# Optimization experiments

Hardware: AMD Instinct MI355X
Metric: run time of the kernel (lower is better)

The kernel has to match this reference:

```python
import jax, jax.numpy as jnp
import numpy as np

KH = KW = 3
PAD = 1
STRIDE = 1
C_IN = 32
C_OUT = 16
H = W = 64
B = 64
H_OUT = (H - KH + 2 * PAD) // STRIDE + 1
W_OUT = (W - KW + 2 * PAD) // STRIDE + 1
S = H_OUT * W_OUT
K = C_IN * KH * KW


def unfold_2d(x):
    # x: [B, C, H, W] -> [B, C*KH*KW, S], torch.nn.functional.unfold ordering
    xp = jnp.pad(x, ((0, 0), (0, 0), (PAD, PAD), (PAD, PAD)))
    patches = []
    for i in range(KH):
        for j in range(KW):
            patches.append(xp[:, :, i:i + H_OUT * STRIDE:STRIDE, j:j + W_OUT * STRIDE:STRIDE])
    u = jnp.stack(patches, axis=2)  # [B, C, KH*KW, H_OUT, W_OUT]
    return u.reshape(x.shape[0], K, S)


def setup_inputs() -> dict:
    key = jax.random.key(0)
    k1, k2, k3 = jax.random.split(key, 3)
    X = jax.random.normal(k1, (B, C_IN, H, W), dtype=jnp.float32)
    # kaiming normal (linear): std = 1/sqrt(fan_in), fan_in = K for each location's GEMM
    weight = jax.random.normal(k2, (S, K, C_OUT), dtype=jnp.float32) / jnp.sqrt(jnp.float32(K))
    # xavier uniform over [H_OUT, W_OUT]
    lim = np.sqrt(6.0 / (H_OUT + W_OUT))
    bias = jax.random.uniform(k3, (H_OUT, W_OUT), dtype=jnp.float32, minval=-lim, maxval=lim)
    return {"X": X, "weight": weight, "bias": bias}


def reference(X, weight, bias):
    ufld = unfold_2d(X)                               # [B, K, S]
    ufld = ufld + bias.reshape(1, 1, -1)              # bias added per-location to patches
    h = jnp.einsum('bks,skc->bcs', ufld, weight)      # per-location unshared GEMM
    return h.reshape(X.shape[0], C_OUT, H_OUT, W_OUT)
```

## Files before the change

### kernel.cpp

```cpp
#include <hip/hip_runtime.h>
#include <stdint.h>
#include <stddef.h>

#define HOUT 64
#define WOUT 64
#define CIN  32
#define COUT 16
#define SLOC 4096
#define KTOT 288
#define HPAD 66
#define WPAD 148

typedef __attribute__((ext_vector_type(8))) short  short8;
typedef __attribute__((ext_vector_type(4))) float  floatx4;
typedef __attribute__((ext_vector_type(2))) float  floatx2;

static __device__ __forceinline__ unsigned short f2bf(float f) {
    union { float f; unsigned int u; } v; v.f = f;
    unsigned int u = v.u;
    unsigned int r = (u + 0x7FFFu + ((u >> 16) & 1u)) >> 16;
    return (unsigned short)r;
}

__global__ __launch_bounds__(256) void prep_kernel(const float* __restrict__ X,
                                                   unsigned short* __restrict__ xt) {
    const int id  = blockIdx.x;
    const int tid = threadIdx.x;

    if (id < 260) {
        int h1, w1;
        if (id < 66)       { h1 = 0;  w1 = id; }
        else if (id < 132) { h1 = 65; w1 = id - 66; }
        else { int r = id - 132; h1 = (r >> 1) + 1; w1 = (r & 1) ? 65 : 0; }
        ((uint4*)(xt + (size_t)(h1 * HPAD + w1) * 2048))[tid] = uint4{0u, 0u, 0u, 0u};
    }

    const int w   = tid >> 2;
    const int cg8 = (tid & 3) * 8;
#pragma unroll
    for (int u = 0; u < 2; ++u) {
        const int unit = id * 2 + u;
        const int h = unit >> 6, b = unit & 63;
        const float* xb = X + (((size_t)b * CIN + cg8) * HOUT + h) * WOUT + w;
        unsigned short v[8];
#pragma unroll
        for (int j = 0; j < 8; ++j)
            v[j] = f2bf(xb[(size_t)j * HOUT * WOUT]);
        uint4 pack;
        pack.x = (unsigned)v[0] | ((unsigned)v[1] << 16);
        pack.y = (unsigned)v[2] | ((unsigned)v[3] << 16);
        pack.z = (unsigned)v[4] | ((unsigned)v[5] << 16);
        pack.w = (unsigned)v[6] | ((unsigned)v[7] << 16);
        *(uint4*)(xt + (size_t)((h + 1) * HPAD + (w + 1)) * 2048 + b * CIN + cg8) = pack;
    }
}

__global__ __launch_bounds__(256, 8) void varconv_kernel(const unsigned short* __restrict__ xt,
                                                         const float* __restrict__ Wg,
                                                         const float* __restrict__ bias,
                                                         float* __restrict__ out) {
    __shared__ __align__(16) unsigned int wru[2][16 * WPAD];
    __shared__ float cs[2][4][16];

    const int id   = blockIdx.x;
    const int sg   = (id & 7) * 256 + (id >> 3);
    const int s0   = sg * 2;
    const int y    = s0 >> 6;
    const int x0   = s0 & 63;
    const int tid  = threadIdx.x;
    const int lane = tid & 63;
    const int wv   = tid >> 6;
    const int q    = lane >> 4;
    const int n    = lane & 15;
    const int B0   = wv * 16;

    const uint4* wsrc = (const uint4*)(Wg + (size_t)s0 * (KTOT * COUT));
    float cacc0[4] = {0.f, 0.f, 0.f, 0.f};
    float cacc1[4] = {0.f, 0.f, 0.f, 0.f};

#define STTASK(T2, SITE, CACC)                                                 \
    {                                                                          \
        const int ng = (T2) & 3, cp = ((T2) >> 2) & 15, t = (T2) >> 6;         \
        const int kA = 18 * cp + t;                                            \
        union { uint4 u; float f[4]; } fA, fB;                                 \
        fA.u = wsrc[(SITE) * 1152 + kA * 4 + ng];                              \
        fB.u = wsrc[(SITE) * 1152 + (kA + 9) * 4 + ng];                        \
        unsigned int* wb = &wru[SITE][0];                                      \
        _Pragma("unroll")                                                      \
        for (int m = 0; m < 4; ++m) {                                          \
            CACC[m] += fA.f[m] + fB.f[m];                                      \
            wb[(4 * ng + m) * WPAD + t * 16 + cp] =                            \
                (unsigned)f2bf(fA.f[m]) | ((unsigned)f2bf(fB.f[m]) << 16);     \
        }                                                                      \
    }

#pragma unroll
    for (int it = 0; it < 5; ++it) {
        const int tau = tid + it * 256;
        if (tau < 576) {
            STTASK(tau, 0, cacc0)
        } else if (tau < 1152) {
            const int t2 = tau - 576;
            STTASK(t2, 1, cacc1)
        }
    }
#undef STTASK

#pragma unroll
    for (int m = 0; m < 4; ++m) {
        cacc0[m] += __shfl_xor(cacc0[m], 4, 64);
        cacc1[m] += __shfl_xor(cacc1[m], 4, 64);
        cacc0[m] += __shfl_xor(cacc0[m], 8, 64);
        cacc1[m] += __shfl_xor(cacc1[m], 8, 64);
        cacc0[m] += __shfl_xor(cacc0[m], 16, 64);
        cacc1[m] += __shfl_xor(cacc1[m], 16, 64);
        cacc0[m] += __shfl_xor(cacc0[m], 32, 64);
        cacc1[m] += __shfl_xor(cacc1[m], 32, 64);
    }
    if (lane < 4) {
#pragma unroll
        for (int m = 0; m < 4; ++m) {
            cs[0][wv][4 * lane + m] = cacc0[m];
            cs[1][wv][4 * lane + m] = cacc1[m];
        }
    }

    __syncthreads();

    floatx4 acc[2];
#pragma unroll
    for (int i = 0; i < 2; ++i) acc[i] = floatx4{0.f, 0.f, 0.f, 0.f};

#define COMPUTE(I)                                                             \
    {                                                                          \
        const int x = x0 + (I);                                                \
        short8 af[9], bf[9];                                                   \
        _Pragma("unroll")                                                      \
        for (int t = 0; t < 9; ++t) {                                          \
            const int cy = t / 3, cx = t % 3;                                  \
            af[t] = *(const short8*)(xt + (size_t)((y + cy) * HPAD + (x + cx)) * 2048 \
                                        + (B0 + n) * CIN + q * 8);             \
        }                                                                      \
        _Pragma("unroll")                                                      \
        for (int t = 0; t < 9; ++t)                                            \
            bf[t] = *(const short8*)&wru[I][n * WPAD + t * 16 + 4 * q];        \
        const float badd = bias[s0 + (I)] * (cs[I][0][n] + cs[I][1][n]        \
                                           + cs[I][2][n] + cs[I][3][n]);       \
        _Pragma("unroll")                                                      \
        for (int t = 0; t < 9; ++t)                                            \
            acc[I] = __builtin_amdgcn_mfma_f32_16x16x32_bf16(af[t], bf[t], acc[I], 0, 0, 0); \
        acc[I][0] += badd; acc[I][1] += badd;                                  \
        acc[I][2] += badd; acc[I][3] += badd;                                  \
    }

    COMPUTE(0)
    COMPUTE(1)
#undef COMPUTE

#pragma unroll
    for (int r = 0; r < 4; ++r) {
        const int b = B0 + 4 * q + r;
        float* dst = out + ((size_t)(b * COUT + n)) * SLOC + s0;
        *(floatx2*)dst = floatx2{acc[0][r], acc[1][r]};
    }
}

extern "C" void kernel_launch(void* const* d_in, const int* in_sizes, int n_in,
                              void* d_out, int out_size, void* d_ws, size_t ws_size,
                              hipStream_t stream) {
    const float* X    = (const float*)d_in[0];
    const float* Wg   = (const float*)d_in[1];
    const float* bias = (const float*)d_in[2];
    float* out = (float*)d_out;

    unsigned short* xt = (unsigned short*)d_ws;

    prep_kernel<<<2048, 256, 0, stream>>>(X, xt);
    varconv_kernel<<<2048, 256, 0, stream>>>(xt, Wg, bias, out);
}
```

Before: 163.3 us.

## Hoist weight and activation loads before LDS staging and share overlapping patches

Issues all global weight loads and the activation patch loads up front, before the fp32-to-bf16 conversion into shared memory and the barrier, so their memory latency overlaps the staging work. The two adjacent output columns now share a 3x4 activation window (12 loads instead of 18), and the two MFMA chains are interleaved. This needs many more live registers, so the launch-bounds occupancy hint drops from 8 to 4 blocks per CU, which could reduce latency hiding across waves.

```diff
diff --git a/kernel.cpp b/kernel.cpp
--- a/kernel.cpp
+++ b/kernel.cpp
@@ -55,7 +55,7 @@
     }
 }
 
-__global__ __launch_bounds__(256, 8) void varconv_kernel(const unsigned short* __restrict__ xt,
+__global__ __launch_bounds__(256, 4) void varconv_kernel(const unsigned short* __restrict__ xt,
                                                          const float* __restrict__ Wg,
                                                          const float* __restrict__ bias,
                                                          float* __restrict__ out) {
@@ -75,36 +75,55 @@
     const int B0   = wv * 16;
 
     const uint4* wsrc = (const uint4*)(Wg + (size_t)s0 * (KTOT * COUT));
+    uint4 fA[5], fB[5];
+#pragma unroll
+    for (int it = 0; it < 5; ++it) {
+        const int tau  = tid + it * 256;
+        const int tt   = tau < 1152 ? tau : 1151;
+        const int site = tt >= 576;
+        const int t2   = tt - 576 * site;
+        const int ng = t2 & 3, cp = (t2 >> 2) & 15, t = t2 >> 6;
+        const int kA = 18 * cp + t;
+        fA[it] = wsrc[site * 1152 + kA * 4 + ng];
+        fB[it] = wsrc[site * 1152 + (kA + 9) * 4 + ng];
+    }
+
+    const unsigned short* abase = xt + (size_t)(B0 + n) * CIN + q * 8;
+    short8 af[3][4];
+#pragma unroll
+    for (int cy = 0; cy < 3; ++cy)
+#pragma unroll
+        for (int cx = 0; cx < 4; ++cx)
+            af[cy][cx] = *(const short8*)(abase + (size_t)((y + cy) * HPAD + (x0 + cx)) * 2048);
+
     float cacc0[4] = {0.f, 0.f, 0.f, 0.f};
     float cacc1[4] = {0.f, 0.f, 0.f, 0.f};
-
-#define STTASK(T2, SITE, CACC)                                                 \
-    {                                                                          \
-        const int ng = (T2) & 3, cp = ((T2) >> 2) & 15, t = (T2) >> 6;         \
-        const int kA = 18 * cp + t;                                            \
-        union { uint4 u; float f[4]; } fA, fB;                                 \
-        fA.u = wsrc[(SITE) * 1152 + kA * 4 + ng];                              \
-        fB.u = wsrc[(SITE) * 1152 + (kA + 9) * 4 + ng];                        \
-        unsigned int* wb = &wru[SITE][0];                                      \
-        _Pragma("unroll")                                                      \
-        for (int m = 0; m < 4; ++m) {                                          \
-            CACC[m] += fA.f[m] + fB.f[m];                                      \
-            wb[(4 * ng + m) * WPAD + t * 16 + cp] =                            \
-                (unsigned)f2bf(fA.f[m]) | ((unsigned)f2bf(fB.f[m]) << 16);     \
-        }                                                                      \
-    }
-
 #pragma unroll
     for (int it = 0; it < 5; ++it) {
         const int tau = tid + it * 256;
-        if (tau < 576) {
-            STTASK(tau, 0, cacc0)
-        } else if (tau < 1152) {
-            const int t2 = tau - 576;
-            STTASK(t2, 1, cacc1)
+        if (tau < 1152) {
+            union { uint4 u; float f[4]; } a, b;
+            a.u = fA[it]; b.u = fB[it];
+            if (tau < 576) {
+                const int ng = tau & 3, cp = (tau >> 2) & 15, t = tau >> 6;
+#pragma unroll
+                for (int m = 0; m < 4; ++m) {
+                    cacc0[m] += a.f[m] + b.f[m];
+                    wru[0][(4 * ng + m) * WPAD + t * 16 + cp] =
+                        (unsigned)f2bf(a.f[m]) | ((unsigned)f2bf(b.f[m]) << 16);
+                }
+            } else {
+                const int t2 = tau - 576;
+                const int ng = t2 & 3, cp = (t2 >> 2) & 15, t = t2 >> 6;
+#pragma unroll
+                for (int m = 0; m < 4; ++m) {
+                    cacc1[m] += a.f[m] + b.f[m];
+                    wru[1][(4 * ng + m) * WPAD + t * 16 + cp] =
+                        (unsigned)f2bf(a.f[m]) | ((unsigned)f2bf(b.f[m]) << 16);
+                }
+            }
         }
     }
-#undef STTASK
 
 #pragma unroll
     for (int m = 0; m < 4; ++m) {
@@ -127,41 +146,26 @@
 
     __syncthreads();
 
-    floatx4 acc[2];
+    floatx4 acc0 = {0.f, 0.f, 0.f, 0.f};
+    floatx4 acc1 = {0.f, 0.f, 0.f, 0.f};
+    const unsigned int* w0 = &wru[0][n * WPAD + 4 * q];
+    const unsigned int* w1 = &wru[1][n * WPAD + 4 * q];
 #pragma unroll
-    for (int i = 0; i < 2; ++i) acc[i] = floatx4{0.f, 0.f, 0.f, 0.f};
-
-#define COMPUTE(I)                                                             \
-    {                                                                          \
-        const int x = x0 + (I);                                                \
-        short8 af[9], bf[9];                                                   \
-        _Pragma("unroll")                                                      \
-        for (int t = 0; t < 9; ++t) {                                          \
-            const int cy = t / 3, cx = t % 3;                                  \
-            af[t] = *(const short8*)(xt + (size_t)((y + cy) * HPAD + (x + cx)) * 2048 \
-                                        + (B0 + n) * CIN + q * 8);             \
-        }                                                                      \
-        _Pragma("unroll")                                                      \
-        for (int t = 0; t < 9; ++t)                                            \
-            bf[t] = *(const short8*)&wru[I][n * WPAD + t * 16 + 4 * q];        \
-        const float badd = bias[s0 + (I)] * (cs[I][0][n] + cs[I][1][n]        \
-                                           + cs[I][2][n] + cs[I][3][n]);       \
-        _Pragma("unroll")                                                      \
-        for (int t = 0; t < 9; ++t)                                            \
-            acc[I] = __builtin_amdgcn_mfma_f32_16x16x32_bf16(af[t], bf[t], acc[I], 0, 0, 0); \
-        acc[I][0] += badd; acc[I][1] += badd;                                  \
-        acc[I][2] += badd; acc[I][3] += badd;                                  \
+    for (int t = 0; t < 9; ++t) {
+        const int cy = t / 3, cx = t % 3;
+        const short8 b0 = *(const short8*)(w0 + t * 16);
+        acc0 = __builtin_amdgcn_mfma_f32_16x16x32_bf16(af[cy][cx], b0, acc0, 0, 0, 0);
+        const short8 b1 = *(const short8*)(w1 + t * 16);
+        acc1 = __builtin_amdgcn_mfma_f32_16x16x32_bf16(af[cy][cx + 1], b1, acc1, 0, 0, 0);
     }
-
-    COMPUTE(0)
-    COMPUTE(1)
-#undef COMPUTE
+    const float badd0 = bias[s0] *     (cs[0][0][n] + cs[0][1][n] + cs[0][2][n] + cs[0][3][n]);
+    const float badd1 = bias[s0 + 1] * (cs[1][0][n] + cs[1][1][n] + cs[1][2][n] + cs[1][3][n]);
 
 #pragma unroll
     for (int r = 0; r < 4; ++r) {
         const int b = B0 + 4 * q + r;
         float* dst = out + ((size_t)(b * COUT + n)) * SLOC + s0;
-        *(floatx2*)dst = floatx2{acc[0][r], acc[1][r]};
+        *(floatx2*)dst = floatx2{acc0[r] + badd0, acc1[r] + badd1};
     }
 }
 
```

After: 155.4 us. 1.05x faster.
